# Kernel optimization log

Hardware: AMD Instinct MI355X
Metric: run time of the kernel (lower is better)

## Reference

```python
import jax, jax.numpy as jnp
import numpy as np

LAYERS = 3       # opt.layer
B = 4096         # batch of sessions
MAX_LEN = 200    # padded session length
N_ITEMS = 100000 # item vocab (index 0 is PAD after zero-row concat)
E = 112          # emb_size (SessConv default)
EPS = 1e-12      # F.normalize eps


def setup_inputs() -> dict:
    key = jax.random.key(0)
    k0, k1, k2, k3, k4 = jax.random.split(key, 5)
    item_embedding = jax.random.normal(k0, (N_ITEMS, E), dtype=jnp.float32) * 0.1
    # Session-session adjacency A and diagonal inverse-degree D (so D @ A is row-normalized)
    A = jax.random.uniform(k1, (B, B), dtype=jnp.float32)
    D = jnp.diag(1.0 / A.sum(axis=1))
    # Padded session item indices; 0 == PAD row (zeros prepended to the table)
    session_item = jax.random.randint(k2, (B, MAX_LEN), 0, N_ITEMS + 1, dtype=jnp.int64)
    session_len = jax.random.randint(k3, (B, 1), 1, MAX_LEN + 1).astype(jnp.float32)
    # layers x Linear(E, E, bias=False) weights, torch layout [out, in]
    Ws = jax.random.normal(k4, (LAYERS, E, E), dtype=jnp.float32) * (1.0 / np.sqrt(E))
    return {"item_embedding": item_embedding, "D": D, "A": A,
            "session_len": session_len, "Ws": Ws, "session_item": session_item}


def reference(item_embedding, D, A, session_len, Ws, session_item):
    # Prepend zero row so index 0 gathers zeros (padding)
    emb = jnp.concatenate([jnp.zeros((1, E), item_embedding.dtype), item_embedding], axis=0)
    # Fused ragged gather + mean-pool (replaces per-session index_select + cpu/numpy roundtrip)
    seq_h = emb[session_item]                       # [B, MAX_LEN, E]
    session_emb = seq_h.sum(axis=1) / session_len   # [B, E]
    DA = D @ A                                      # [B, B]
    acc = session_emb                               # layer-0 term of the final average
    for i in range(LAYERS):
        session_emb = session_emb @ Ws[i].T         # Linear(E,E,bias=False)
        session_emb = DA @ session_emb              # session graph propagation
        nrm = jnp.linalg.norm(session_emb, axis=-1, keepdims=True)
        acc = acc + session_emb / jnp.maximum(nrm, EPS)  # appended term is L2-normalized
        # NOTE: next layer consumes the UN-normalized session_emb (as in the torch code)
    return acc / (LAYERS + 1)
```

## Files before the change

### kernel.cpp

```cpp
#include <hip/hip_runtime.h>
#include <hip/hip_bf16.h>

#define BSZ 4096
#define MAXLEN 200
#define EDIM 112

typedef __attribute__((ext_vector_type(8))) short bf16x8;
typedef __attribute__((ext_vector_type(4))) float f32x4;

static __device__ __forceinline__ short f2bf(float f) {
    unsigned u = __float_as_uint(f);
    unsigned r = (u + 0x7fffu + ((u >> 16) & 1u)) >> 16;
    return (short)r;
}
static __device__ __forceinline__ float bf2f(short s) {
    return __uint_as_float(((unsigned)(unsigned short)s) << 16);
}
static __device__ __forceinline__ bf16x8 cvt8(float4 a, float4 b) {
    bf16x8 r;
    r[0] = f2bf(a.x); r[1] = f2bf(a.y); r[2] = f2bf(a.z); r[3] = f2bf(a.w);
    r[4] = f2bf(b.x); r[5] = f2bf(b.y); r[6] = f2bf(b.z); r[7] = f2bf(b.w);
    return r;
}
static __device__ __forceinline__ unsigned pack2(float a, float b) {
    return ((unsigned)f2bf(a) & 0xffffu) | ((unsigned)f2bf(b) << 16);
}

__global__ __launch_bounds__(256) void f32_to_bf16(const float* __restrict__ src,
                                                   unsigned short* __restrict__ dst,
                                                   int ngroups, int zgroups) {
    int g = blockIdx.x * 256 + threadIdx.x;
    if (g >= ngroups) return;
    bf16x8 o;
    if (g < zgroups) {
        #pragma unroll
        for (int i = 0; i < 8; ++i) o[i] = 0;
    } else {
        const float* p = src + (size_t)(g - zgroups) * 8;
        float4 a = *(const float4*)p;
        float4 b = *(const float4*)(p + 4);
        o = cvt8(a, b);
    }
    *(bf16x8*)(dst + (size_t)g * 8) = o;
}

__global__ __launch_bounds__(256) void gather_pool_bf(const unsigned short* __restrict__ Ebf,
                                                      const int* __restrict__ items,
                                                      const float* __restrict__ slen,
                                                      float* __restrict__ S,
                                                      float* __restrict__ acc) {
    __shared__ float part[16][14][8];
    int wave = threadIdx.x >> 6;
    int lane = threadIdx.x & 63;
    int b = blockIdx.x;
    int rg = lane / 14;
    int c  = lane % 14;
    const int* it = items + (size_t)b * MAXLEN + wave * 50;
    float a[8];
    #pragma unroll
    for (int e = 0; e < 8; ++e) a[e] = 0.f;
    if (lane < 56) {
        #pragma unroll
        for (int t = 0; t < 13; ++t) {
            int j = t * 4 + rg;
            int idx = 0;
            if (j < 50) idx = it[j];
            bf16x8 v = *(const bf16x8*)(Ebf + (size_t)idx * EDIM + c * 8);
            #pragma unroll
            for (int e = 0; e < 8; ++e) a[e] += bf2f(v[e]);
        }
        #pragma unroll
        for (int e = 0; e < 8; ++e) part[wave * 4 + rg][c][e] = a[e];
    }
    __syncthreads();
    int tid = threadIdx.x;
    if (tid < EDIM) {
        int cc = tid >> 3, ee = tid & 7;
        float s = 0.f;
        #pragma unroll
        for (int g = 0; g < 16; ++g) s += part[g][cc][ee];
        s /= slen[b];
        S[(size_t)b * EDIM + tid]   = s;
        acc[(size_t)b * EDIM + tid] = s;
    }
}

static __device__ __forceinline__ bf16x8 ldcvt(const float* p, bool valid) {
    if (valid) {
        float4 a = *(const float4*)p;
        float4 b = *(const float4*)(p + 4);
        return cvt8(a, b);
    }
    bf16x8 z;
    #pragma unroll
    for (int i = 0; i < 8; ++i) z[i] = 0;
    return z;
}

template <int MODE>
__global__ __launch_bounds__(256) void fused_mid(const float* __restrict__ Sin,
                                                 const float* __restrict__ Yp,
                                                 const float* __restrict__ Dm,
                                                 float* __restrict__ accb,
                                                 const float* __restrict__ W,
                                                 unsigned short* __restrict__ Bsw) {
    __shared__ unsigned short Ylds[4][16][136];
    int wave = threadIdx.x >> 6;
    int lane = threadIdx.x & 63;
    int gw = blockIdx.x * 4 + wave;
    int j0 = gw * 16;
    int nrow = lane & 15;
    int quad = lane >> 4;
    int ses = j0 + nrow;

    float4 v[7];
    if (MODE == 0) {
        const float4* p = (const float4*)(Sin + (size_t)ses * EDIM + quad * 28);
        #pragma unroll
        for (int i = 0; i < 7; ++i) v[i] = p[i];
    } else {
        #pragma unroll
        for (int i = 0; i < 7; ++i) v[i] = make_float4(0.f, 0.f, 0.f, 0.f);
        #pragma unroll
        for (int pp = 0; pp < 4; ++pp) {
            const float4* p = (const float4*)(Yp + (size_t)pp * BSZ * EDIM
                                              + (size_t)ses * EDIM + quad * 28);
            #pragma unroll
            for (int i = 0; i < 7; ++i) {
                float4 t = p[i];
                v[i].x += t.x; v[i].y += t.y; v[i].z += t.z; v[i].w += t.w;
            }
        }
        float d = Dm[(size_t)ses * (BSZ + 1)];
        float ss = 0.f;
        #pragma unroll
        for (int i = 0; i < 7; ++i) {
            v[i].x *= d; v[i].y *= d; v[i].z *= d; v[i].w *= d;
            ss += v[i].x * v[i].x + v[i].y * v[i].y + v[i].z * v[i].z + v[i].w * v[i].w;
        }
        ss += __shfl_xor(ss, 16, 64);
        ss += __shfl_xor(ss, 32, 64);
        float rinv = 1.f / fmaxf(sqrtf(ss), 1e-12f);
        float4* pa = (float4*)(accb + (size_t)ses * EDIM + quad * 28);
        #pragma unroll
        for (int i = 0; i < 7; ++i) {
            float4 a = pa[i];
            a.x += v[i].x * rinv; a.y += v[i].y * rinv;
            a.z += v[i].z * rinv; a.w += v[i].w * rinv;
            pa[i] = a;
        }
    }

    #pragma unroll
    for (int i = 0; i < 7; ++i) {
        uint2 pk;
        pk.x = pack2(v[i].x, v[i].y);
        pk.y = pack2(v[i].z, v[i].w);
        *(uint2*)&Ylds[wave][nrow][quad * 28 + i * 4] = pk;
    }
    *(uint2*)&Ylds[wave][nrow][112 + quad * 4] = make_uint2(0u, 0u);
    __syncthreads();

    bf16x8 aF[4];
    #pragma unroll
    for (int k32 = 0; k32 < 4; ++k32)
        aF[k32] = *(bf16x8*)&Ylds[wave][nrow][k32 * 32 + quad * 8];

    f32x4 acc[7];
    #pragma unroll
    for (int t = 0; t < 7; ++t) acc[t] = (f32x4){0.f, 0.f, 0.f, 0.f};
    #pragma unroll
    for (int t = 0; t < 7; ++t) {
        const float* wr = W + (size_t)(16 * t + nrow) * EDIM;
        #pragma unroll
        for (int k32 = 0; k32 < 4; ++k32) {
            bf16x8 bF = ldcvt(wr + k32 * 32 + quad * 8, (k32 < 3) || (quad < 2));
            acc[t] = __builtin_amdgcn_mfma_f32_16x16x32_bf16(aF[k32], bF, acc[t], 0, 0, 0);
        }
    }

    int k32f = j0 >> 5;
    int qp = ((j0 >> 4) & 1) * 2 + (quad >> 1);
    int e0 = (quad & 1) * 4;
    #pragma unroll
    for (int t = 0; t < 7; ++t) {
        uint2 pk;
        pk.x = pack2(acc[t][0], acc[t][1]);
        pk.y = pack2(acc[t][2], acc[t][3]);
        *(uint2*)(Bsw + ((size_t)(k32f * 7 + t) * 64 + qp * 16 + nrow) * 8 + e0) = pk;
    }
}

template <int AMODE>
__global__ __launch_bounds__(256) void big_gemm(const float* __restrict__ Af,
                                                unsigned short* __restrict__ Asw,
                                                const unsigned short* __restrict__ Bsw,
                                                float* __restrict__ Yp) {
    __shared__ float red[4][16][113];

    int wave = threadIdx.x >> 6;
    int lane = threadIdx.x & 63;
    int mtile = blockIdx.x & 255;
    int kc = blockIdx.x >> 8;
    int m0 = mtile * 16;
    int nrow = lane & 15;
    int quad = lane >> 4;

    f32x4 acc[7];
    #pragma unroll
    for (int t = 0; t < 7; ++t) acc[t] = (f32x4){0.f, 0.f, 0.f, 0.f};

    for (int ks = 0; ks < 8; ++ks) {
        int k32 = kc * 32 + wave * 8 + ks;
        bf16x8 aF;
        size_t afrag = ((size_t)(mtile * 128 + k32) * 64 + lane) * 8;
        if (AMODE == 0) {
            const float* p = Af + (size_t)(m0 + nrow) * 4096 + k32 * 32 + quad * 8;
            float4 a0 = *(const float4*)p;
            float4 a1 = *(const float4*)(p + 4);
            aF = cvt8(a0, a1);
            *(bf16x8*)(Asw + afrag) = aF;
        } else {
            aF = *(const bf16x8*)(Asw + afrag);
        }
        const unsigned short* bb = Bsw + ((size_t)k32 * 7 * 64 + lane) * 8;
        #pragma unroll
        for (int t = 0; t < 7; ++t) {
            bf16x8 bF = *(const bf16x8*)(bb + (size_t)t * 512);
            acc[t] = __builtin_amdgcn_mfma_f32_16x16x32_bf16(aF, bF, acc[t], 0, 0, 0);
        }
    }

    #pragma unroll
    for (int t = 0; t < 7; ++t)
        #pragma unroll
        for (int r = 0; r < 4; ++r)
            red[wave][quad * 4 + r][16 * t + nrow] = acc[t][r];
    __syncthreads();

    float* dst = Yp + (size_t)kc * BSZ * EDIM;
    for (int e = threadIdx.x; e < 16 * EDIM; e += 256) {
        int r = e / EDIM, c = e % EDIM;
        float s = red[0][r][c] + red[1][r][c] + red[2][r][c] + red[3][r][c];
        dst[(size_t)(m0 + r) * EDIM + c] = s;
    }
}

__global__ __launch_bounds__(256) void final_epilogue(const float* __restrict__ Yp,
                                                      const float* __restrict__ Dm,
                                                      const float* __restrict__ accb,
                                                      float* __restrict__ out) {
    int wave = threadIdx.x >> 6;
    int lane = threadIdx.x & 63;
    int b = blockIdx.x * 4 + wave;

    float2 v = make_float2(0.f, 0.f);
    size_t o2 = (size_t)b * 56 + lane;
    if (lane < 56) {
        #pragma unroll
        for (int p = 0; p < 4; ++p) {
            float2 t = ((const float2*)(Yp + (size_t)p * BSZ * EDIM))[o2];
            v.x += t.x;
            v.y += t.y;
        }
    }
    float d = Dm[(size_t)b * (BSZ + 1)];
    v.x *= d; v.y *= d;
    float ss = v.x * v.x + v.y * v.y;
    #pragma unroll
    for (int off = 32; off; off >>= 1) ss += __shfl_xor(ss, off, 64);
    float nrm = fmaxf(sqrtf(ss), 1e-12f);
    if (lane < 56) {
        float2 a = ((const float2*)accb)[o2];
        ((float2*)out)[o2] = make_float2((a.x + v.x / nrm) * 0.25f,
                                         (a.y + v.y / nrm) * 0.25f);
    }
}

extern "C" void kernel_launch(void* const* d_in, const int* in_sizes, int n_in,
                              void* d_out, int out_size, void* d_ws, size_t ws_size,
                              hipStream_t stream) {
    (void)in_sizes; (void)n_in; (void)out_size; (void)ws_size;
    const float* emb   = (const float*)d_in[0];
    const float* Dm    = (const float*)d_in[1];
    const float* A     = (const float*)d_in[2];
    const float* slen  = (const float*)d_in[3];
    const float* Ws    = (const float*)d_in[4];
    const int*   items = (const int*)d_in[5];
    float* out = (float*)d_out;

    char* w = (char*)d_ws;
    float* Sa   = (float*)w;
    float* accb = Sa + BSZ * EDIM;
    float* Yp   = accb + BSZ * EDIM;
    unsigned short* Bsw = (unsigned short*)(Yp + 4 * BSZ * EDIM);
    unsigned short* Ebf = Bsw + 128 * 7 * 64 * 8;
    unsigned short* Asw = Ebf + 100001 * EDIM;

    f32_to_bf16<<<5470, 256, 0, stream>>>(emb, Ebf, 1400014, 14);
    gather_pool_bf<<<BSZ, 256, 0, stream>>>(Ebf, items, slen, Sa, accb);
    fused_mid<0><<<64, 256, 0, stream>>>(Sa, nullptr, nullptr, nullptr, Ws, Bsw);
    big_gemm<0><<<1024, 256, 0, stream>>>(A, Asw, Bsw, Yp);
    fused_mid<1><<<64, 256, 0, stream>>>(nullptr, Yp, Dm, accb,
                                         Ws + (size_t)EDIM * EDIM, Bsw);
    big_gemm<1><<<1024, 256, 0, stream>>>(nullptr, Asw, Bsw, Yp);
    fused_mid<1><<<64, 256, 0, stream>>>(nullptr, Yp, Dm, accb,
                                         Ws + (size_t)2 * EDIM * EDIM, Bsw);
    big_gemm<1><<<1024, 256, 0, stream>>>(nullptr, Asw, Bsw, Yp);
    final_epilogue<<<BSZ / 4, 256, 0, stream>>>(Yp, Dm, accb, out);
}
```

Before: 292.0 us.

## Use single-wave GEMM blocks with two M-tiles and 16-way split-K partials

The big GEMM moves from 4-wave blocks that reduce partial sums through LDS to single-wave blocks. Each block covers two 16-row M tiles so every B fragment load feeds two MFMAs, and partial results are written straight to 16 split-K buffers instead of 4. The aim is to drop the LDS reduction and barrier and to halve B traffic per MFMA. In exchange, the downstream mid and final kernels must sum 16 partial buffers instead of 4, which adds global memory reads and workspace.

```diff
diff --git a/kernel.cpp b/kernel.cpp
--- a/kernel.cpp
+++ b/kernel.cpp
@@ -4,6 +4,7 @@
 #define BSZ 4096
 #define MAXLEN 200
 #define EDIM 112
+#define NKC 16
 
 typedef __attribute__((ext_vector_type(8))) short bf16x8;
 typedef __attribute__((ext_vector_type(4))) float f32x4;
@@ -98,16 +99,15 @@
 }
 
 template <int MODE>
-__global__ __launch_bounds__(256) void fused_mid(const float* __restrict__ Sin,
-                                                 const float* __restrict__ Yp,
-                                                 const float* __restrict__ Dm,
-                                                 float* __restrict__ accb,
-                                                 const float* __restrict__ W,
-                                                 unsigned short* __restrict__ Bsw) {
-    __shared__ unsigned short Ylds[4][16][136];
-    int wave = threadIdx.x >> 6;
-    int lane = threadIdx.x & 63;
-    int gw = blockIdx.x * 4 + wave;
+__global__ __launch_bounds__(64, 4) void fused_mid(const float* __restrict__ Sin,
+                                                   const float* __restrict__ Yp,
+                                                   const float* __restrict__ Dm,
+                                                   float* __restrict__ accb,
+                                                   const float* __restrict__ W,
+                                                   unsigned short* __restrict__ Bsw) {
+    __shared__ unsigned short Ylds[16][136];
+    int lane = threadIdx.x;
+    int gw = blockIdx.x;
     int j0 = gw * 16;
     int nrow = lane & 15;
     int quad = lane >> 4;
@@ -121,8 +121,8 @@
     } else {
         #pragma unroll
         for (int i = 0; i < 7; ++i) v[i] = make_float4(0.f, 0.f, 0.f, 0.f);
-        #pragma unroll
-        for (int pp = 0; pp < 4; ++pp) {
+        #pragma unroll 4
+        for (int pp = 0; pp < NKC; ++pp) {
             const float4* p = (const float4*)(Yp + (size_t)pp * BSZ * EDIM
                                               + (size_t)ses * EDIM + quad * 28);
             #pragma unroll
@@ -156,15 +156,15 @@
         uint2 pk;
         pk.x = pack2(v[i].x, v[i].y);
         pk.y = pack2(v[i].z, v[i].w);
-        *(uint2*)&Ylds[wave][nrow][quad * 28 + i * 4] = pk;
-    }
-    *(uint2*)&Ylds[wave][nrow][112 + quad * 4] = make_uint2(0u, 0u);
+        *(uint2*)&Ylds[nrow][quad * 28 + i * 4] = pk;
+    }
+    *(uint2*)&Ylds[nrow][112 + quad * 4] = make_uint2(0u, 0u);
     __syncthreads();
 
     bf16x8 aF[4];
     #pragma unroll
     for (int k32 = 0; k32 < 4; ++k32)
-        aF[k32] = *(bf16x8*)&Ylds[wave][nrow][k32 * 32 + quad * 8];
+        aF[k32] = *(bf16x8*)&Ylds[nrow][k32 * 32 + quad * 8];
 
     f32x4 acc[7];
     #pragma unroll
@@ -192,58 +192,56 @@
 }
 
 template <int AMODE>
-__global__ __launch_bounds__(256) void big_gemm(const float* __restrict__ Af,
-                                                unsigned short* __restrict__ Asw,
-                                                const unsigned short* __restrict__ Bsw,
-                                                float* __restrict__ Yp) {
-    __shared__ float red[4][16][113];
-
-    int wave = threadIdx.x >> 6;
-    int lane = threadIdx.x & 63;
-    int mtile = blockIdx.x & 255;
-    int kc = blockIdx.x >> 8;
-    int m0 = mtile * 16;
+__global__ __launch_bounds__(64, 4) void big_gemm(const float* __restrict__ Af,
+                                                  unsigned short* __restrict__ Asw,
+                                                  const unsigned short* __restrict__ Bsw,
+                                                  float* __restrict__ Yp) {
+    int lane = threadIdx.x;
+    int mt2 = blockIdx.x & 127;
+    int kc = blockIdx.x >> 7;
     int nrow = lane & 15;
     int quad = lane >> 4;
 
-    f32x4 acc[7];
-    #pragma unroll
-    for (int t = 0; t < 7; ++t) acc[t] = (f32x4){0.f, 0.f, 0.f, 0.f};
+    f32x4 acc[2][7];
+    #pragma unroll
+    for (int s = 0; s < 2; ++s)
+        #pragma unroll
+        for (int t = 0; t < 7; ++t) acc[s][t] = (f32x4){0.f, 0.f, 0.f, 0.f};
 
     for (int ks = 0; ks < 8; ++ks) {
-        int k32 = kc * 32 + wave * 8 + ks;
-        bf16x8 aF;
-        size_t afrag = ((size_t)(mtile * 128 + k32) * 64 + lane) * 8;
-        if (AMODE == 0) {
-            const float* p = Af + (size_t)(m0 + nrow) * 4096 + k32 * 32 + quad * 8;
-            float4 a0 = *(const float4*)p;
-            float4 a1 = *(const float4*)(p + 4);
-            aF = cvt8(a0, a1);
-            *(bf16x8*)(Asw + afrag) = aF;
-        } else {
-            aF = *(const bf16x8*)(Asw + afrag);
+        int k32 = kc * 8 + ks;
+        bf16x8 aF[2];
+        #pragma unroll
+        for (int sub = 0; sub < 2; ++sub) {
+            int mtile = mt2 * 2 + sub;
+            size_t afrag = ((size_t)(mtile * 128 + k32) * 64 + lane) * 8;
+            if (AMODE == 0) {
+                const float* p = Af + (size_t)(mtile * 16 + nrow) * 4096 + k32 * 32 + quad * 8;
+                float4 a0 = *(const float4*)p;
+                float4 a1 = *(const float4*)(p + 4);
+                aF[sub] = cvt8(a0, a1);
+                *(bf16x8*)(Asw + afrag) = aF[sub];
+            } else {
+                aF[sub] = *(const bf16x8*)(Asw + afrag);
+            }
         }
         const unsigned short* bb = Bsw + ((size_t)k32 * 7 * 64 + lane) * 8;
         #pragma unroll
         for (int t = 0; t < 7; ++t) {
             bf16x8 bF = *(const bf16x8*)(bb + (size_t)t * 512);
-            acc[t] = __builtin_amdgcn_mfma_f32_16x16x32_bf16(aF, bF, acc[t], 0, 0, 0);
-        }
-    }
-
-    #pragma unroll
-    for (int t = 0; t < 7; ++t)
-        #pragma unroll
-        for (int r = 0; r < 4; ++r)
-            red[wave][quad * 4 + r][16 * t + nrow] = acc[t][r];
-    __syncthreads();
-
-    float* dst = Yp + (size_t)kc * BSZ * EDIM;
-    for (int e = threadIdx.x; e < 16 * EDIM; e += 256) {
-        int r = e / EDIM, c = e % EDIM;
-        float s = red[0][r][c] + red[1][r][c] + red[2][r][c] + red[3][r][c];
-        dst[(size_t)(m0 + r) * EDIM + c] = s;
-    }
+            acc[0][t] = __builtin_amdgcn_mfma_f32_16x16x32_bf16(aF[0], bF, acc[0][t], 0, 0, 0);
+            acc[1][t] = __builtin_amdgcn_mfma_f32_16x16x32_bf16(aF[1], bF, acc[1][t], 0, 0, 0);
+        }
+    }
+
+    float* dst = Yp + (size_t)kc * BSZ * EDIM + (size_t)mt2 * 32 * EDIM;
+    #pragma unroll
+    for (int sub = 0; sub < 2; ++sub)
+        #pragma unroll
+        for (int t = 0; t < 7; ++t)
+            #pragma unroll
+            for (int r = 0; r < 4; ++r)
+                dst[(size_t)(sub * 16 + quad * 4 + r) * EDIM + 16 * t + nrow] = acc[sub][t][r];
 }
 
 __global__ __launch_bounds__(256) void final_epilogue(const float* __restrict__ Yp,
@@ -257,8 +255,8 @@
     float2 v = make_float2(0.f, 0.f);
     size_t o2 = (size_t)b * 56 + lane;
     if (lane < 56) {
-        #pragma unroll
-        for (int p = 0; p < 4; ++p) {
+        #pragma unroll 4
+        for (int p = 0; p < NKC; ++p) {
             float2 t = ((const float2*)(Yp + (size_t)p * BSZ * EDIM))[o2];
             v.x += t.x;
             v.y += t.y;
@@ -293,19 +291,19 @@
     float* Sa   = (float*)w;
     float* accb = Sa + BSZ * EDIM;
     float* Yp   = accb + BSZ * EDIM;
-    unsigned short* Bsw = (unsigned short*)(Yp + 4 * BSZ * EDIM);
+    unsigned short* Bsw = (unsigned short*)(Yp + (size_t)NKC * BSZ * EDIM);
     unsigned short* Ebf = Bsw + 128 * 7 * 64 * 8;
     unsigned short* Asw = Ebf + 100001 * EDIM;
 
     f32_to_bf16<<<5470, 256, 0, stream>>>(emb, Ebf, 1400014, 14);
     gather_pool_bf<<<BSZ, 256, 0, stream>>>(Ebf, items, slen, Sa, accb);
-    fused_mid<0><<<64, 256, 0, stream>>>(Sa, nullptr, nullptr, nullptr, Ws, Bsw);
-    big_gemm<0><<<1024, 256, 0, stream>>>(A, Asw, Bsw, Yp);
-    fused_mid<1><<<64, 256, 0, stream>>>(nullptr, Yp, Dm, accb,
+    fused_mid<0><<<256, 64, 0, stream>>>(Sa, nullptr, nullptr, nullptr, Ws, Bsw);
+    big_gemm<0><<<2048, 64, 0, stream>>>(A, Asw, Bsw, Yp);
+    fused_mid<1><<<256, 64, 0, stream>>>(nullptr, Yp, Dm, accb,
                                          Ws + (size_t)EDIM * EDIM, Bsw);
-    big_gemm<1><<<1024, 256, 0, stream>>>(nullptr, Asw, Bsw, Yp);
-    fused_mid<1><<<64, 256, 0, stream>>>(nullptr, Yp, Dm, accb,
+    big_gemm<1><<<2048, 64, 0, stream>>>(nullptr, Asw, Bsw, Yp);
+    fused_mid<1><<<256, 64, 0, stream>>>(nullptr, Yp, Dm, accb,
                                          Ws + (size_t)2 * EDIM * EDIM, Bsw);
-    big_gemm<1><<<1024, 256, 0, stream>>>(nullptr, Asw, Bsw, Yp);
+    big_gemm<1><<<2048, 64, 0, stream>>>(nullptr, Asw, Bsw, Yp);
     final_epilogue<<<BSZ / 4, 256, 0, stream>>>(Yp, Dm, accb, out);
 }
```

Measured after the change: 287.9 us. About the same (-1.4%).
